# Kernel tuning notes

Measured on AMD Instinct MI355X. Metric: run time of the kernel, lower is better.

## Reference

```python
import jax, jax.numpy as jnp
import numpy as np

H = 128   # LSTM hidden size
E = 300   # embedding dim
PAD_ID = 0
UNK_ID = 1


def _lstm_dir(x, Wih, Whh, b):
    """Single-direction LSTM. x: [B,S,E] -> hidden states [B,S,H]. PyTorch gate order i,f,g,o."""
    B = x.shape[0]
    def step(carry, xt):
        h, c = carry
        g = xt @ Wih.T + h @ Whh.T + b            # [B,4H]
        i, f, gg, o = jnp.split(g, 4, axis=-1)
        c = jax.nn.sigmoid(f) * c + jax.nn.sigmoid(i) * jnp.tanh(gg)
        h = jax.nn.sigmoid(o) * jnp.tanh(c)
        return (h, c), h
    init = (jnp.zeros((B, H), x.dtype), jnp.zeros((B, H), x.dtype))
    _, hs = jax.lax.scan(step, init, jnp.swapaxes(x, 0, 1))   # [S,B,H]
    return jnp.swapaxes(hs, 0, 1)


def setup_inputs() -> dict:
    key = jax.random.key(0)
    ks = jax.random.split(key, 12)
    B, S, D = 32, 512, 8
    WORD_V, DEP_V, NUM_LABELS = 100000, 64, 5
    inp = {
        "word_ids": jax.random.randint(ks[0], (B, 3, S), 0, WORD_V, dtype=jnp.int32),
        "deps_ids": jax.random.randint(ks[1], (B, S, D), 0, DEP_V, dtype=jnp.int32),
        "word_table": jax.random.normal(ks[2], (WORD_V, E), jnp.float32) * 0.1,
        "dep_table": jax.random.normal(ks[3], (DEP_V, E), jnp.float32) * 0.1,
        "Wih_f": jax.random.normal(ks[4], (4 * H, E), jnp.float32) * 0.05,
        "Whh_f": jax.random.normal(ks[5], (4 * H, H), jnp.float32) * 0.05,
        "b_f": jnp.zeros((4 * H,), jnp.float32),
        "Wih_b": jax.random.normal(ks[6], (4 * H, E), jnp.float32) * 0.05,
        "Whh_b": jax.random.normal(ks[7], (4 * H, H), jnp.float32) * 0.05,
        "b_b": jnp.zeros((4 * H,), jnp.float32),
        "W_cls": jax.random.normal(ks[8], (NUM_LABELS, 2 * H), jnp.float32) * 0.05,
        "b_cls": jnp.zeros((NUM_LABELS,), jnp.float32),
    }
    return inp


def reference(word_ids, deps_ids, word_table, dep_table,
              Wih_f, Whh_f, b_f, Wih_b, Whh_b, b_b, W_cls, b_cls):
    # word_ids[:, 1, :] -> token ids used for word embeddings
    word_embs = word_table[word_ids[:, 1, :]]          # [B,S,E]
    dep_embs = dep_table[deps_ids]                     # [B,S,D,E]

    # vectorized masked mean-pool of dep embeddings (skip pad/unk ids)
    mask = ((deps_ids != PAD_ID) & (deps_ids != UNK_ID)).astype(word_embs.dtype)[..., None]  # [B,S,D,1]
    cnt = mask.sum(axis=2)                             # [B,S,1]
    dep_mean = (dep_embs * mask).sum(axis=2) / jnp.maximum(cnt, 1.0)
    word_embs = jnp.where(cnt > 0, 0.5 * word_embs + 0.5 * dep_mean, word_embs)

    # BiLSTM
    out_f = _lstm_dir(word_embs, Wih_f, Whh_f, b_f)                       # [B,S,H]
    out_b = _lstm_dir(word_embs[:, ::-1, :], Wih_b, Whh_b, b_b)[:, ::-1, :]
    out = jnp.concatenate([out_f, out_b], axis=-1)                        # [B,S,2H]

    # max-pool over time, dropout is identity in eval, then classifier
    pooled = out.max(axis=1)                           # [B,2H]
    logits = pooled @ W_cls.T + b_cls                  # [B,num_labels]
    return logits
```

## Files before the change

### kernel.cpp

```cpp
#include <hip/hip_runtime.h>
#include <hip/hip_bf16.h>
#include <cstdint>
#include <cstddef>

#define S_LEN 512
#define BATCH 32
#define EDIM  300
#define KPAD  320
#define HDIM  128
#define NGATE 512
#define NCOLS 1024

typedef float    f2   __attribute__((ext_vector_type(2)));
typedef float    f4v  __attribute__((ext_vector_type(4)));
typedef _Float16 h2   __attribute__((ext_vector_type(2)));
typedef _Float16 half8 __attribute__((ext_vector_type(8)));

__device__ __forceinline__ h2 pk_f16(float a, float b) {
    auto r = __builtin_amdgcn_cvt_pkrtz(a, b);
    return __builtin_bit_cast(h2, r);
}

__global__ void embed_wcat(const int* __restrict__ word_ids,
                           const int* __restrict__ deps_ids,
                           const float* __restrict__ word_table,
                           const float* __restrict__ dep_table,
                           const float* __restrict__ Wih_f,
                           const float* __restrict__ Wih_b,
                           _Float16* __restrict__ Xcat,
                           _Float16* __restrict__ Wcat) {
    int blk = blockIdx.x;
    if (blk >= BATCH * S_LEN) {
        int n = blk - BATCH * S_LEN;
        const float* src = (n < NGATE) ? (Wih_f + (size_t)n * EDIM)
                                       : (Wih_b + (size_t)(n - NGATE) * EDIM);
        _Float16* wr = Wcat + (size_t)n * KPAD;
        for (int e = threadIdx.x; e < KPAD; e += 128)
            wr[e] = (_Float16)((e < EDIM) ? src[e] : 0.f);
        return;
    }
    int pos = blk;
    int b = pos >> 9, s = pos & (S_LEN - 1);
    int wid = word_ids[b * 3 * S_LEN + S_LEN + s];
    const int* dp = deps_ids + (size_t)pos * 8;
    int ids[8];
    int cnt = 0;
#pragma unroll
    for (int d = 0; d < 8; ++d) {
        int id = dp[d];
        ids[d] = id;
        cnt += (id != 0 && id != 1) ? 1 : 0;
    }
    float inv = 0.5f / (float)((cnt > 0) ? cnt : 1);
    const float* wr = word_table + (size_t)wid * EDIM;
    _Float16* xr = Xcat + (size_t)pos * KPAD;
    for (int e = threadIdx.x; e < KPAD; e += 128) {
        float v = 0.f;
        if (e < EDIM) {
            float w = wr[e];
            float dsum = 0.f;
#pragma unroll
            for (int d = 0; d < 8; ++d) {
                if (ids[d] != 0 && ids[d] != 1) dsum += dep_table[ids[d] * EDIM + e];
            }
            v = (cnt > 0) ? (0.5f * w + dsum * inv) : w;
        }
        xr[e] = (_Float16)v;
    }
}

#define LSTR 40
__global__ __launch_bounds__(256) void gemm_mfma(
        const _Float16* __restrict__ Xcat,
        const _Float16* __restrict__ Wcat,
        const float* __restrict__ b_f, const float* __restrict__ b_b,
        float* __restrict__ pre) {
    __shared__ _Float16 Asub[128 * LSTR];
    __shared__ _Float16 Bsub[128 * LSTR];
    int tid = threadIdx.x;
    int wave = tid >> 6, lane = tid & 63;
    int lid = lane & 15, quad = lane >> 4;
    int m0 = blockIdx.x * 128, n0 = blockIdx.y * 128;
    int wm = (wave >> 1) * 64, wn = (wave & 1) * 64;

    f4v acc[4][4];
#pragma unroll
    for (int i = 0; i < 4; ++i)
#pragma unroll
        for (int j = 0; j < 4; ++j) acc[i][j] = (f4v)0.f;

    float bias[4];
#pragma unroll
    for (int nt = 0; nt < 4; ++nt) {
        int n = n0 + wn + nt * 16 + lid;
        bias[nt] = (n < NGATE) ? b_f[n] : b_b[n - NGATE];
    }

    int c0 = tid, c1 = tid + 256;
    const _Float16* aptr0 = Xcat + (size_t)(m0 + (c0 >> 2)) * KPAD + (c0 & 3) * 8;
    const _Float16* aptr1 = Xcat + (size_t)(m0 + (c1 >> 2)) * KPAD + (c1 & 3) * 8;
    const _Float16* bptr0 = Wcat + (size_t)(n0 + (c0 >> 2)) * KPAD + (c0 & 3) * 8;
    const _Float16* bptr1 = Wcat + (size_t)(n0 + (c1 >> 2)) * KPAD + (c1 & 3) * 8;
    int la0 = (c0 >> 2) * LSTR + (c0 & 3) * 8;
    int la1 = (c1 >> 2) * LSTR + (c1 & 3) * 8;

    half8 ra0 = *(const half8*)(aptr0);
    half8 ra1 = *(const half8*)(aptr1);
    half8 rb0 = *(const half8*)(bptr0);
    half8 rb1 = *(const half8*)(bptr1);

    for (int k0 = 0; k0 < KPAD; k0 += 32) {
        __syncthreads();
        *(half8*)&Asub[la0] = ra0;
        *(half8*)&Asub[la1] = ra1;
        *(half8*)&Bsub[la0] = rb0;
        *(half8*)&Bsub[la1] = rb1;
        __syncthreads();
        if (k0 + 32 < KPAD) {
            ra0 = *(const half8*)(aptr0 + k0 + 32);
            ra1 = *(const half8*)(aptr1 + k0 + 32);
            rb0 = *(const half8*)(bptr0 + k0 + 32);
            rb1 = *(const half8*)(bptr1 + k0 + 32);
        }
        half8 aF[4], bF[4];
#pragma unroll
        for (int mt = 0; mt < 4; ++mt)
            aF[mt] = *(const half8*)&Asub[(wm + mt * 16 + lid) * LSTR + quad * 8];
#pragma unroll
        for (int nt = 0; nt < 4; ++nt)
            bF[nt] = *(const half8*)&Bsub[(wn + nt * 16 + lid) * LSTR + quad * 8];
#pragma unroll
        for (int mt = 0; mt < 4; ++mt)
#pragma unroll
            for (int nt = 0; nt < 4; ++nt)
                acc[mt][nt] = __builtin_amdgcn_mfma_f32_16x16x32_f16(
                    aF[mt], bF[nt], acc[mt][nt], 0, 0, 0);
    }

#pragma unroll
    for (int mt = 0; mt < 4; ++mt)
#pragma unroll
        for (int nt = 0; nt < 4; ++nt) {
            int n = n0 + wn + nt * 16 + lid;
#pragma unroll
            for (int r = 0; r < 4; ++r) {
                int m = m0 + wm + mt * 16 + quad * 4 + r;
                pre[(size_t)m * NCOLS + n] = acc[mt][nt][r] + bias[nt];
            }
        }
}

__global__ __launch_bounds__(256, 1) void lstm_rec(
        const float* __restrict__ pre,
        const float* __restrict__ Whh_f, const float* __restrict__ Whh_b,
        float* __restrict__ pooled) {
    __shared__ _Float16 h_s[HDIM];
    int t = threadIdx.x;
    int lane = t & 63;
    int wv = t >> 6;
    int tau = lane & 3;
    int ks  = (lane >> 2) & 3;
    int hi2 = lane >> 4;
    int hbase = wv * 32 + hi2 * 8;
    int b = blockIdx.x >> 1;
    int dir = blockIdx.x & 1;
    const float* Whh = dir ? Whh_b : Whh_f;

    h2 w[8][16];
#pragma unroll
    for (int j = 0; j < 8; ++j) {
        const float* rp = Whh + (size_t)(tau * HDIM + hbase + j) * HDIM + ks * 32;
#pragma unroll
        for (int q = 0; q < 16; ++q) w[j][q] = pk_f16(rp[2 * q], rp[2 * q + 1]);
    }

    float c = 0.f;
    float hmax = -1e30f;
    if (t < 64) ((uint*)h_s)[t] = 0u;

    const float* pX = pre + (size_t)b * S_LEN * NCOLS + dir * NGATE
                    + tau * HDIM + hbase + 2 * ks;
    const float* pY = pX + 1;
    int s = dir ? (S_LEN - 1) : 0;
    int sd = dir ? -1 : 1;
    float pXn1 = pX[(long)s * NCOLS], pYn1 = pY[(long)s * NCOLS];
    float pXn2 = pX[(long)(s + sd) * NCOLS], pYn2 = pY[(long)(s + sd) * NCOLS];

    int hZ = hbase + 2 * ks + (tau >> 1);
    bool is_g = (tau == 2);
    float mult = is_g ? -2.f : -1.f;
    float sA   = is_g ?  2.f :  1.f;
    float sB   = is_g ? -1.f :  0.f;
    bool oy = (tau & 2) != 0;
    const h2* hp = (const h2*)h_s + ks * 16;

    asm volatile("s_waitcnt lgkmcnt(0)\n\ts_barrier" ::: "memory");

    for (int step = 0; step < S_LEN; ++step) {
        float curX = pXn1, curY = pYn1;
        pXn1 = pXn2; pYn1 = pYn2;
        if (step + 2 < S_LEN) {
            pXn2 = pX[(long)(s + 2 * sd) * NCOLS];
            pYn2 = pY[(long)(s + 2 * sd) * NCOLS];
        }

        h2 hh[16];
#pragma unroll
        for (int q = 0; q < 16; ++q) hh[q] = hp[q];

        float P[8];
#pragma unroll
        for (int j = 0; j < 8; ++j) {
            float acc = 0.f;
#pragma unroll
            for (int q = 0; q < 16; ++q)
                acc = __builtin_amdgcn_fdot2(w[j][q], hh[q], acc, false);
            P[j] = acc;
        }

        float R0 = P[0], R1 = P[1], R2 = P[2], R3 = P[3];
        float R4 = P[4], R5 = P[5], R6 = P[6], R7 = P[7];
        asm("s_nop 1\n\t"
            "v_add_f32_dpp %0, %0, %0 row_ror:4 row_mask:0xf bank_mask:0xf\n\t"
            "v_add_f32_dpp %1, %1, %1 row_ror:4 row_mask:0xf bank_mask:0xf\n\t"
            "v_add_f32_dpp %2, %2, %2 row_ror:4 row_mask:0xf bank_mask:0xf\n\t"
            "v_add_f32_dpp %3, %3, %3 row_ror:4 row_mask:0xf bank_mask:0xf\n\t"
            "v_add_f32_dpp %4, %4, %4 row_ror:4 row_mask:0xf bank_mask:0xf\n\t"
            "v_add_f32_dpp %5, %5, %5 row_ror:4 row_mask:0xf bank_mask:0xf\n\t"
            "v_add_f32_dpp %6, %6, %6 row_ror:4 row_mask:0xf bank_mask:0xf\n\t"
            "v_add_f32_dpp %7, %7, %7 row_ror:4 row_mask:0xf bank_mask:0xf\n\t"
            "v_add_f32_dpp %0, %0, %0 row_ror:8 row_mask:0xf bank_mask:0xf\n\t"
            "v_add_f32_dpp %1, %1, %1 row_ror:8 row_mask:0xf bank_mask:0xf\n\t"
            "v_add_f32_dpp %2, %2, %2 row_ror:8 row_mask:0xf bank_mask:0xf\n\t"
            "v_add_f32_dpp %3, %3, %3 row_ror:8 row_mask:0xf bank_mask:0xf\n\t"
            "v_add_f32_dpp %4, %4, %4 row_ror:8 row_mask:0xf bank_mask:0xf\n\t"
            "v_add_f32_dpp %5, %5, %5 row_ror:8 row_mask:0xf bank_mask:0xf\n\t"
            "v_add_f32_dpp %6, %6, %6 row_ror:8 row_mask:0xf bank_mask:0xf\n\t"
            "v_add_f32_dpp %7, %7, %7 row_ror:8 row_mask:0xf bank_mask:0xf"
            : "+v"(R0), "+v"(R1), "+v"(R2), "+v"(R3),
              "+v"(R4), "+v"(R5), "+v"(R6), "+v"(R7));

        float X01 = (ks & 1) ? R2 : R0;
        float X23 = (ks & 1) ? R6 : R4;
        float X   = (ks & 2) ? X23 : X01;
        float Y01 = (ks & 1) ? R3 : R1;
        float Y23 = (ks & 1) ? R7 : R5;
        float Y   = (ks & 2) ? Y23 : Y01;
        float gX = X + curX;
        float gY = Y + curY;

        float eX = __expf(gX * mult);
        float eY = __expf(gY * mult);
        float rX = __builtin_amdgcn_rcpf(1.f + eX);
        float rY = __builtin_amdgcn_rcpf(1.f + eY);
        float actX = fmaf(rX, sA, sB);
        float actY = fmaf(rY, sA, sB);

        float aiX, afX, agX, aoX, aiY, afY, agY, aoY;
        asm("s_nop 1\n\t"
            "v_mov_b32_dpp %0, %8 quad_perm:[0,0,0,0] row_mask:0xf bank_mask:0xf\n\t"
            "v_mov_b32_dpp %4, %9 quad_perm:[0,0,0,0] row_mask:0xf bank_mask:0xf\n\t"
            "v_mov_b32_dpp %1, %8 quad_perm:[1,1,1,1] row_mask:0xf bank_mask:0xf\n\t"
            "v_mov_b32_dpp %5, %9 quad_perm:[1,1,1,1] row_mask:0xf bank_mask:0xf\n\t"
            "v_mov_b32_dpp %2, %8 quad_perm:[2,2,2,2] row_mask:0xf bank_mask:0xf\n\t"
            "v_mov_b32_dpp %6, %9 quad_perm:[2,2,2,2] row_mask:0xf bank_mask:0xf\n\t"
            "v_mov_b32_dpp %3, %8 quad_perm:[3,3,3,3] row_mask:0xf bank_mask:0xf\n\t"
            "v_mov_b32_dpp %7, %9 quad_perm:[3,3,3,3] row_mask:0xf bank_mask:0xf"
            : "=&v"(aiX), "=&v"(afX), "=&v"(agX), "=&v"(aoX),
              "=&v"(aiY), "=&v"(afY), "=&v"(agY), "=&v"(aoY)
            : "v"(actX), "v"(actY));

        float ai = oy ? aiY : aiX;
        float af = oy ? afY : afX;
        float ag = oy ? agY : agX;
        float ao = oy ? aoY : aoX;

        c = fmaf(af, c, ai * ag);
        float ec = __expf(-2.f * c);
        float rc = __builtin_amdgcn_rcpf(1.f + ec);
        float h  = ao * fmaf(rc, 2.f, -1.f);
        hmax = fmaxf(hmax, h);

        if ((tau & 1) == 0) h_s[hZ] = (_Float16)h;
        asm volatile("s_waitcnt lgkmcnt(0)\n\ts_barrier" ::: "memory");
        s += sd;
    }

    if ((tau & 1) == 0) pooled[b * 256 + dir * HDIM + hZ] = hmax;
}

__global__ void cls_kernel(const float* __restrict__ pooled,
                           const float* __restrict__ W_cls,
                           const float* __restrict__ b_cls,
                           float* __restrict__ out) {
    int i = threadIdx.x;
    if (i < BATCH * 5) {
        int b = i / 5, l = i % 5;
        float acc = b_cls[l];
        const float* p = pooled + b * 256;
        const float* w = W_cls + l * 256;
#pragma unroll 8
        for (int j = 0; j < 256; ++j) acc = fmaf(p[j], w[j], acc);
        out[i] = acc;
    }
}

extern "C" void kernel_launch(void* const* d_in, const int* in_sizes, int n_in,
                              void* d_out, int out_size, void* d_ws, size_t ws_size,
                              hipStream_t stream) {
    const int*   word_ids   = (const int*)d_in[0];
    const int*   deps_ids   = (const int*)d_in[1];
    const float* word_table = (const float*)d_in[2];
    const float* dep_table  = (const float*)d_in[3];
    const float* Wih_f      = (const float*)d_in[4];
    const float* Whh_f      = (const float*)d_in[5];
    const float* b_f        = (const float*)d_in[6];
    const float* Wih_b      = (const float*)d_in[7];
    const float* Whh_b      = (const float*)d_in[8];
    const float* b_b        = (const float*)d_in[9];
    const float* W_cls      = (const float*)d_in[10];
    const float* b_cls      = (const float*)d_in[11];
    float* out = (float*)d_out;

    float*     pre    = (float*)d_ws;
    float*     pooled = pre + (size_t)BATCH * S_LEN * NCOLS;
    _Float16*  Xcat   = (_Float16*)(pooled + BATCH * 256);
    _Float16*  Wcat   = Xcat + (size_t)BATCH * S_LEN * KPAD;

    embed_wcat<<<BATCH * S_LEN + NCOLS, 128, 0, stream>>>(
        word_ids, deps_ids, word_table, dep_table, Wih_f, Wih_b, Xcat, Wcat);
    gemm_mfma<<<dim3(128, 8), 256, 0, stream>>>(Xcat, Wcat, b_f, b_b, pre);
    lstm_rec<<<64, 256, 0, stream>>>(pre, Whh_f, Whh_b, pooled);
    cls_kernel<<<1, 192, 0, stream>>>(pooled, W_cls, b_cls, out);
}
```

Measured before the change: 485.0 us.

## Batch 16 sequences per block and run LSTM recurrence with MFMA

```diff
diff --git a/kernel.cpp b/kernel.cpp
--- a/kernel.cpp
+++ b/kernel.cpp
@@ -14,12 +14,8 @@
 typedef float    f2   __attribute__((ext_vector_type(2)));
 typedef float    f4v  __attribute__((ext_vector_type(4)));
 typedef _Float16 h2   __attribute__((ext_vector_type(2)));
+typedef _Float16 h4   __attribute__((ext_vector_type(4)));
 typedef _Float16 half8 __attribute__((ext_vector_type(8)));
-
-__device__ __forceinline__ h2 pk_f16(float a, float b) {
-    auto r = __builtin_amdgcn_cvt_pkrtz(a, b);
-    return __builtin_bit_cast(h2, r);
-}
 
 __global__ void embed_wcat(const int* __restrict__ word_ids,
                            const int* __restrict__ deps_ids,
@@ -150,143 +146,128 @@
         }
 }
 
-__global__ __launch_bounds__(256, 1) void lstm_rec(
+#define HSTR 304
+__global__ __launch_bounds__(512, 2) void lstm_rec(
         const float* __restrict__ pre,
         const float* __restrict__ Whh_f, const float* __restrict__ Whh_b,
         float* __restrict__ pooled) {
-    __shared__ _Float16 h_s[HDIM];
+    __shared__ __align__(16) _Float16 Hs[2 * 16 * (HSTR / 2)];
     int t = threadIdx.x;
     int lane = t & 63;
     int wv = t >> 6;
-    int tau = lane & 3;
-    int ks  = (lane >> 2) & 3;
-    int hi2 = lane >> 4;
-    int hbase = wv * 32 + hi2 * 8;
-    int b = blockIdx.x >> 1;
-    int dir = blockIdx.x & 1;
+    int lid = lane & 15;
+    int quad = lane >> 4;
+    int dir = blockIdx.x >> 1;
+    int b = (blockIdx.x & 1) * 16 + lid;
     const float* Whh = dir ? Whh_b : Whh_f;
 
-    h2 w[8][16];
-#pragma unroll
-    for (int j = 0; j < 8; ++j) {
-        const float* rp = Whh + (size_t)(tau * HDIM + hbase + j) * HDIM + ks * 32;
-#pragma unroll
-        for (int q = 0; q < 16; ++q) w[j][q] = pk_f16(rp[2 * q], rp[2 * q + 1]);
-    }
-
-    float c = 0.f;
-    float hmax = -1e30f;
-    if (t < 64) ((uint*)h_s)[t] = 0u;
-
-    const float* pX = pre + (size_t)b * S_LEN * NCOLS + dir * NGATE
-                    + tau * HDIM + hbase + 2 * ks;
-    const float* pY = pX + 1;
-    int s = dir ? (S_LEN - 1) : 0;
-    int sd = dir ? -1 : 1;
-    float pXn1 = pX[(long)s * NCOLS], pYn1 = pY[(long)s * NCOLS];
-    float pXn2 = pX[(long)(s + sd) * NCOLS], pYn2 = pY[(long)(s + sd) * NCOLS];
-
-    int hZ = hbase + 2 * ks + (tau >> 1);
-    bool is_g = (tau == 2);
-    float mult = is_g ? -2.f : -1.f;
-    float sA   = is_g ?  2.f :  1.f;
-    float sB   = is_g ? -1.f :  0.f;
-    bool oy = (tau & 2) != 0;
-    const h2* hp = (const h2*)h_s + ks * 16;
+    half8 afr[4][4];
+#pragma unroll
+    for (int tau = 0; tau < 4; ++tau)
+#pragma unroll
+        for (int kt = 0; kt < 4; ++kt) {
+            const float* rp = Whh + (size_t)(tau * HDIM + 16 * wv + lid) * HDIM
+                            + 32 * kt + 8 * quad;
+            half8 hv;
+#pragma unroll
+            for (int e = 0; e < 8; ++e) hv[e] = (_Float16)rp[e];
+            afr[tau][kt] = hv;
+        }
+
+    for (int i = t; i < 2 * 16 * (HSTR / 4); i += 512) ((uint*)Hs)[i] = 0u;
+
+    const char* hrd0 = (const char*)Hs + lid * HSTR + 16 * quad;
+    const char* hrd1 = hrd0 + 16 * HSTR;
+    char* hwr0 = (char*)Hs + lid * HSTR + (16 * wv + 4 * quad) * 2;
+    char* hwr1 = hwr0 + 16 * HSTR;
+
+    const f4v zero4 = (f4v)0.f;
+    float cc[4] = {0.f, 0.f, 0.f, 0.f};
+    float hm[4] = {-1e30f, -1e30f, -1e30f, -1e30f};
+
+    int s0 = dir ? (S_LEN - 1) : 0;
+    long pstride = dir ? -(long)NCOLS : (long)NCOLS;
+    const float* pf = pre + (size_t)(b * S_LEN + s0) * NCOLS + dir * NGATE
+                    + 16 * wv + 4 * quad;
+
+    float pnA[16], pnB[16];
+#pragma unroll
+    for (int j = 0; j < 16; ++j) pnA[j] = pf[(j >> 2) * HDIM + (j & 3)];
+    pf += pstride;
+#pragma unroll
+    for (int j = 0; j < 16; ++j) pnB[j] = pf[(j >> 2) * HDIM + (j & 3)];
+    pf += pstride;
 
     asm volatile("s_waitcnt lgkmcnt(0)\n\ts_barrier" ::: "memory");
 
-    for (int step = 0; step < S_LEN; ++step) {
-        float curX = pXn1, curY = pYn1;
-        pXn1 = pXn2; pYn1 = pYn2;
-        if (step + 2 < S_LEN) {
-            pXn2 = pX[(long)(s + 2 * sd) * NCOLS];
-            pYn2 = pY[(long)(s + 2 * sd) * NCOLS];
-        }
-
-        h2 hh[16];
-#pragma unroll
-        for (int q = 0; q < 16; ++q) hh[q] = hp[q];
-
-        float P[8];
-#pragma unroll
-        for (int j = 0; j < 8; ++j) {
-            float acc = 0.f;
-#pragma unroll
-            for (int q = 0; q < 16; ++q)
-                acc = __builtin_amdgcn_fdot2(w[j][q], hh[q], acc, false);
-            P[j] = acc;
-        }
-
-        float R0 = P[0], R1 = P[1], R2 = P[2], R3 = P[3];
-        float R4 = P[4], R5 = P[5], R6 = P[6], R7 = P[7];
-        asm("s_nop 1\n\t"
-            "v_add_f32_dpp %0, %0, %0 row_ror:4 row_mask:0xf bank_mask:0xf\n\t"
-            "v_add_f32_dpp %1, %1, %1 row_ror:4 row_mask:0xf bank_mask:0xf\n\t"
-            "v_add_f32_dpp %2, %2, %2 row_ror:4 row_mask:0xf bank_mask:0xf\n\t"
-            "v_add_f32_dpp %3, %3, %3 row_ror:4 row_mask:0xf bank_mask:0xf\n\t"
-            "v_add_f32_dpp %4, %4, %4 row_ror:4 row_mask:0xf bank_mask:0xf\n\t"
-            "v_add_f32_dpp %5, %5, %5 row_ror:4 row_mask:0xf bank_mask:0xf\n\t"
-            "v_add_f32_dpp %6, %6, %6 row_ror:4 row_mask:0xf bank_mask:0xf\n\t"
-            "v_add_f32_dpp %7, %7, %7 row_ror:4 row_mask:0xf bank_mask:0xf\n\t"
-            "v_add_f32_dpp %0, %0, %0 row_ror:8 row_mask:0xf bank_mask:0xf\n\t"
-            "v_add_f32_dpp %1, %1, %1 row_ror:8 row_mask:0xf bank_mask:0xf\n\t"
-            "v_add_f32_dpp %2, %2, %2 row_ror:8 row_mask:0xf bank_mask:0xf\n\t"
-            "v_add_f32_dpp %3, %3, %3 row_ror:8 row_mask:0xf bank_mask:0xf\n\t"
-            "v_add_f32_dpp %4, %4, %4 row_ror:8 row_mask:0xf bank_mask:0xf\n\t"
-            "v_add_f32_dpp %5, %5, %5 row_ror:8 row_mask:0xf bank_mask:0xf\n\t"
-            "v_add_f32_dpp %6, %6, %6 row_ror:8 row_mask:0xf bank_mask:0xf\n\t"
-            "v_add_f32_dpp %7, %7, %7 row_ror:8 row_mask:0xf bank_mask:0xf"
-            : "+v"(R0), "+v"(R1), "+v"(R2), "+v"(R3),
-              "+v"(R4), "+v"(R5), "+v"(R6), "+v"(R7));
-
-        float X01 = (ks & 1) ? R2 : R0;
-        float X23 = (ks & 1) ? R6 : R4;
-        float X   = (ks & 2) ? X23 : X01;
-        float Y01 = (ks & 1) ? R3 : R1;
-        float Y23 = (ks & 1) ? R7 : R5;
-        float Y   = (ks & 2) ? Y23 : Y01;
-        float gX = X + curX;
-        float gY = Y + curY;
-
-        float eX = __expf(gX * mult);
-        float eY = __expf(gY * mult);
-        float rX = __builtin_amdgcn_rcpf(1.f + eX);
-        float rY = __builtin_amdgcn_rcpf(1.f + eY);
-        float actX = fmaf(rX, sA, sB);
-        float actY = fmaf(rY, sA, sB);
-
-        float aiX, afX, agX, aoX, aiY, afY, agY, aoY;
-        asm("s_nop 1\n\t"
-            "v_mov_b32_dpp %0, %8 quad_perm:[0,0,0,0] row_mask:0xf bank_mask:0xf\n\t"
-            "v_mov_b32_dpp %4, %9 quad_perm:[0,0,0,0] row_mask:0xf bank_mask:0xf\n\t"
-            "v_mov_b32_dpp %1, %8 quad_perm:[1,1,1,1] row_mask:0xf bank_mask:0xf\n\t"
-            "v_mov_b32_dpp %5, %9 quad_perm:[1,1,1,1] row_mask:0xf bank_mask:0xf\n\t"
-            "v_mov_b32_dpp %2, %8 quad_perm:[2,2,2,2] row_mask:0xf bank_mask:0xf\n\t"
-            "v_mov_b32_dpp %6, %9 quad_perm:[2,2,2,2] row_mask:0xf bank_mask:0xf\n\t"
-            "v_mov_b32_dpp %3, %8 quad_perm:[3,3,3,3] row_mask:0xf bank_mask:0xf\n\t"
-            "v_mov_b32_dpp %7, %9 quad_perm:[3,3,3,3] row_mask:0xf bank_mask:0xf"
-            : "=&v"(aiX), "=&v"(afX), "=&v"(agX), "=&v"(aoX),
-              "=&v"(aiY), "=&v"(afY), "=&v"(agY), "=&v"(aoY)
-            : "v"(actX), "v"(actY));
-
-        float ai = oy ? aiY : aiX;
-        float af = oy ? afY : afX;
-        float ag = oy ? agY : agX;
-        float ao = oy ? aoY : aoX;
-
-        c = fmaf(af, c, ai * ag);
-        float ec = __expf(-2.f * c);
-        float rc = __builtin_amdgcn_rcpf(1.f + ec);
-        float h  = ao * fmaf(rc, 2.f, -1.f);
-        hmax = fmaxf(hmax, h);
-
-        if ((tau & 1) == 0) h_s[hZ] = (_Float16)h;
-        asm volatile("s_waitcnt lgkmcnt(0)\n\ts_barrier" ::: "memory");
-        s += sd;
-    }
-
-    if ((tau & 1) == 0) pooled[b * 256 + dir * HDIM + hZ] = hmax;
+#define LSTM_STEP(PN, HRD, HWR, DOLOAD)                                       \
+    do {                                                                      \
+        half8 bf0 = *(const half8*)(HRD);                                     \
+        half8 bf1 = *(const half8*)(HRD + 64);                                \
+        half8 bf2 = *(const half8*)(HRD + 128);                               \
+        half8 bf3 = *(const half8*)(HRD + 192);                               \
+        f4v acc[4];                                                           \
+        _Pragma("unroll")                                                     \
+        for (int tau = 0; tau < 4; ++tau) {                                   \
+            f4v a = __builtin_amdgcn_mfma_f32_16x16x32_f16(                   \
+                afr[tau][0], bf0, zero4, 0, 0, 0);                            \
+            a = __builtin_amdgcn_mfma_f32_16x16x32_f16(                       \
+                afr[tau][1], bf1, a, 0, 0, 0);                                \
+            a = __builtin_amdgcn_mfma_f32_16x16x32_f16(                       \
+                afr[tau][2], bf2, a, 0, 0, 0);                                \
+            a = __builtin_amdgcn_mfma_f32_16x16x32_f16(                       \
+                afr[tau][3], bf3, a, 0, 0, 0);                                \
+            acc[tau] = a;                                                     \
+        }                                                                     \
+        float g[4][4];                                                        \
+        _Pragma("unroll")                                                     \
+        for (int tau = 0; tau < 4; ++tau)                                     \
+            _Pragma("unroll")                                                 \
+            for (int r = 0; r < 4; ++r)                                       \
+                g[tau][r] = acc[tau][r] + PN[tau * 4 + r];                    \
+        if (DOLOAD) {                                                         \
+            _Pragma("unroll")                                                 \
+            for (int j = 0; j < 16; ++j)                                      \
+                PN[j] = pf[(j >> 2) * HDIM + (j & 3)];                        \
+        }                                                                     \
+        pf += pstride;                                                        \
+        float hv[4];                                                          \
+        _Pragma("unroll")                                                     \
+        for (int r = 0; r < 4; ++r) {                                         \
+            float ei = __expf(-g[0][r]);                                      \
+            float ii = __builtin_amdgcn_rcpf(1.f + ei);                       \
+            float ef = __expf(-g[1][r]);                                      \
+            float ff = __builtin_amdgcn_rcpf(1.f + ef);                       \
+            float eg = __expf(-2.f * g[2][r]);                                \
+            float tg = fmaf(__builtin_amdgcn_rcpf(1.f + eg), 2.f, -1.f);      \
+            float eo = __expf(-g[3][r]);                                      \
+            float oo = __builtin_amdgcn_rcpf(1.f + eo);                       \
+            cc[r] = fmaf(ff, cc[r], ii * tg);                                 \
+            float et = __expf(-2.f * cc[r]);                                  \
+            float th = fmaf(__builtin_amdgcn_rcpf(1.f + et), 2.f, -1.f);      \
+            float hh = oo * th;                                               \
+            hm[r] = fmaxf(hm[r], hh);                                         \
+            hv[r] = hh;                                                       \
+        }                                                                     \
+        h4 hwv;                                                               \
+        hwv[0] = (_Float16)hv[0];                                             \
+        hwv[1] = (_Float16)hv[1];                                             \
+        hwv[2] = (_Float16)hv[2];                                             \
+        hwv[3] = (_Float16)hv[3];                                             \
+        *(h4*)(HWR) = hwv;                                                    \
+        asm volatile("s_waitcnt lgkmcnt(0)\n\ts_barrier" ::: "memory");       \
+    } while (0)
+
+    for (int i = 0; i < S_LEN / 2; ++i) {
+        bool doload = (i < S_LEN / 2 - 1);
+        LSTM_STEP(pnA, hrd0, hwr1, doload);
+        LSTM_STEP(pnB, hrd1, hwr0, doload);
+    }
+#undef LSTM_STEP
+
+#pragma unroll
+    for (int r = 0; r < 4; ++r)
+        pooled[b * 256 + dir * HDIM + 16 * wv + 4 * quad + r] = hm[r];
 }
 
 __global__ void cls_kernel(const float* __restrict__ pooled,
@@ -330,6 +311,6 @@
     embed_wcat<<<BATCH * S_LEN + NCOLS, 128, 0, stream>>>(
         word_ids, deps_ids, word_table, dep_table, Wih_f, Wih_b, Xcat, Wcat);
     gemm_mfma<<<dim3(128, 8), 256, 0, stream>>>(Xcat, Wcat, b_f, b_b, pre);
-    lstm_rec<<<64, 256, 0, stream>>>(pre, Whh_f, Whh_b, pooled);
+    lstm_rec<<<4, 512, 0, stream>>>(pre, Whh_f, Whh_b, pooled);
     cls_kernel<<<1, 192, 0, stream>>>(pooled, W_cls, b_cls, out);
 }
```

Result: slower. 769.4 us (+58.6%).
